# Kernel tuning notes

Measured on AMD Instinct MI355X. Metric: run time of the kernel, lower is better.

## Reference

```python
import jax, jax.numpy as jnp
import numpy as np

B = 8
N_PER = 8192   # xyz points per batch
M_PER = 2048   # query points per batch
C_FEAT = 32
RADIUS = 0.2
K = 32         # sample_nums
USE_XYZ = True


def setup_inputs() -> dict:
    key = jax.random.key(0)
    k1, k2, k3 = jax.random.split(key, 3)
    xyz = jax.random.uniform(k1, (B * N_PER, 3), dtype=jnp.float32)
    new_xyz = jax.random.uniform(k2, (B * M_PER, 3), dtype=jnp.float32)
    features = jax.random.normal(k3, (B * N_PER, C_FEAT), dtype=jnp.float32)
    xyz_batch_cnt = jnp.full((B,), N_PER, dtype=jnp.int32)
    new_xyz_batch_cnt = jnp.full((B,), M_PER, dtype=jnp.int32)
    return {
        "xyz": xyz,
        "xyz_batch_cnt": xyz_batch_cnt,
        "new_xyz": new_xyz,
        "new_xyz_batch_cnt": new_xyz_batch_cnt,
        "features": features,
    }


def _ball_query(xyz_b, new_b, radius, k):
    # xyz_b: (B, N, 3), new_b: (B, M, 3)
    n = xyz_b.shape[1]
    # squared pairwise distances (B, M, N)
    d2 = jnp.sum((new_b[:, :, None, :] - xyz_b[:, None, :, :]) ** 2, axis=-1)
    mask = d2 < (radius * radius)
    # first-k in-radius indices (CUDA ball_query keeps neighbors in point order)
    scores = jnp.where(mask, jnp.arange(n, dtype=jnp.int32), jnp.int32(n))
    idx_sorted = jnp.sort(scores, axis=-1)[..., :k]          # (B, M, k)
    cnt = jnp.sum(mask, axis=-1)                              # (B, M)
    empty = cnt == 0                                          # (B, M)
    first = idx_sorted[..., :1]                               # duplicate first hit
    slot = jnp.arange(k, dtype=jnp.int32)
    idx = jnp.where(slot[None, None, :] < cnt[..., None], idx_sorted, first)
    idx = jnp.where(empty[..., None], jnp.int32(0), idx)      # empty balls -> 0
    return idx, empty


def reference(xyz, xyz_batch_cnt, new_xyz, new_xyz_batch_cnt, features):
    b = xyz_batch_cnt.shape[0]
    xyz_b = xyz.reshape(b, -1, 3)          # (B, N, 3)
    new_b = new_xyz.reshape(b, -1, 3)      # (B, M, 3)
    feat_b = features.reshape(b, xyz_b.shape[1], -1)  # (B, N, C)

    idx, empty = _ball_query(xyz_b, new_b, RADIUS, K)  # (B, M, K), (B, M)

    gather = jax.vmap(lambda pts, i: pts[i])           # per-batch gather
    grouped_xyz = gather(xyz_b, idx) - new_b[:, :, None, :]   # (B, M, K, 3)
    grouped_xyz = jnp.where(empty[..., None, None], 0.0, grouped_xyz)

    grouped_feat = gather(feat_b, idx)                        # (B, M, K, C)
    grouped_feat = jnp.where(empty[..., None, None], 0.0, grouped_feat)

    if USE_XYZ:
        new_features = jnp.concatenate([grouped_xyz, grouped_feat], axis=-1)
    else:
        new_features = grouped_feat
    # (B, M, K, 3+C) -> (B*M, 3+C, K) to match torch (Mtot, C', nsample)
    m_tot = b * new_b.shape[1]
    new_features = jnp.transpose(new_features, (0, 1, 3, 2)).reshape(
        m_tot, -1, K)
    idx_flat = idx.reshape(m_tot, K)
    return new_features, idx_flat
```

## Files before the change

### kernel.cpp

```cpp
#include <hip/hip_runtime.h>

#define BATCHES   8
#define N_PER     8192
#define M_PER     2048
#define C_FEAT    32
#define KNN       32
#define R2        0.04f
#define M_TOT     (BATCHES * M_PER)
#define FEAT_OUT  (3 + C_FEAT)
#define OUT_FEAT_SZ ((size_t)M_TOT * FEAT_OUT * KNN)

__global__ __launch_bounds__(256) void sqag_fused_kernel(
    const float* __restrict__ xyz,
    const float* __restrict__ new_xyz,
    const float* __restrict__ features,
    float* __restrict__ out)
{
    __shared__ int sidx[4][KNN];

    const int wave = threadIdx.x >> 6;
    const int lane = threadIdx.x & 63;

    const int bswz   = blockIdx.x & 7;
    const int within = blockIdx.x >> 3;
    const int q = __builtin_amdgcn_readfirstlane(
        (bswz * (M_PER / 4) + within) * 4 + wave);
    const int b    = q >> 11;
    const int base = b * N_PER;

    const float px = new_xyz[q * 3 + 0];
    const float py = new_xyz[q * 3 + 1];
    const float pz = new_xyz[q * 3 + 2];

    int cnt = 0;
    int first = 0;

    float cx[4], cy[4], cz[4];
    const float* p = xyz + (size_t)base * 3 + lane * 3;
    #pragma unroll
    for (int c = 0; c < 4; ++c) {
        cx[c] = p[c * 192 + 0];
        cy[c] = p[c * 192 + 1];
        cz[c] = p[c * 192 + 2];
    }

    for (int cb = 0;;) {
        const bool more = (cb + 256) < N_PER;
        float nx[4], ny[4], nz[4];
        if (more) {
            const float* pn = p + 768;
            #pragma unroll
            for (int c = 0; c < 4; ++c) {
                nx[c] = pn[c * 192 + 0];
                ny[c] = pn[c * 192 + 1];
                nz[c] = pn[c * 192 + 2];
            }
        }

        unsigned long long m[4];
        bool in[4];
        #pragma unroll
        for (int c = 0; c < 4; ++c) {
            const float dx = px - cx[c];
            const float dy = py - cy[c];
            const float dz = pz - cz[c];
            const float d2 = __fadd_rn(__fadd_rn(__fmul_rn(dx, dx),
                                                 __fmul_rn(dy, dy)),
                                       __fmul_rn(dz, dz));
            in[c] = d2 < R2;
            m[c]  = __ballot(in[c]);
        }

        if (cnt == 0) {
            if      (m[0]) first = cb +       (__ffsll((long long)m[0]) - 1);
            else if (m[1]) first = cb +  64 + (__ffsll((long long)m[1]) - 1);
            else if (m[2]) first = cb + 128 + (__ffsll((long long)m[2]) - 1);
            else if (m[3]) first = cb + 192 + (__ffsll((long long)m[3]) - 1);
        }

        int pre = cnt;
        #pragma unroll
        for (int c = 0; c < 4; ++c) {
            if (in[c]) {
                const int r = pre + (int)__builtin_amdgcn_mbcnt_hi(
                    (unsigned)(m[c] >> 32),
                    __builtin_amdgcn_mbcnt_lo((unsigned)m[c], 0u));
                if (r < KNN) sidx[wave][r] = cb + c * 64 + lane;
            }
            pre += __popcll(m[c]);
        }
        cnt = pre;

        if (cnt >= KNN || !more) break;
        p += 768;
        cb += 256;
        #pragma unroll
        for (int c = 0; c < 4; ++c) {
            cx[c] = nx[c]; cy[c] = ny[c]; cz[c] = nz[c];
        }
    }

    const int pad = (cnt == 0) ? 0 : first;
    if (lane >= cnt && lane < KNN) sidx[wave][lane] = pad;
    const float zf = (cnt == 0) ? 0.0f : 1.0f;

    const int k    = lane & 31;
    const int half = lane >> 5;

    const int li = sidx[wave][k];
    const int gi = base + li;

    const float4* f = (const float4*)(features + (size_t)gi * C_FEAT + half * 16);
    const float4 v0 = f[0];
    const float4 v1 = f[1];
    const float4 v2 = f[2];
    const float4 v3 = f[3];

    const float gx = xyz[(size_t)gi * 3 + 0] - px;
    const float gy = xyz[(size_t)gi * 3 + 1] - py;
    const float gz = xyz[(size_t)gi * 3 + 2] - pz;

    float* o = out + (size_t)q * (FEAT_OUT * KNN);
    if (half == 0) {
        __builtin_nontemporal_store(zf * gx, &o[0 * KNN + k]);
        __builtin_nontemporal_store(zf * gy, &o[1 * KNN + k]);
        __builtin_nontemporal_store(zf * gz, &o[2 * KNN + k]);
        __builtin_nontemporal_store((float)li,
                                    &out[OUT_FEAT_SZ + (size_t)q * KNN + k]);
    }

    const int jb = 3 + half * 16;
    __builtin_nontemporal_store(zf * v0.x, &o[(jb +  0) * KNN + k]);
    __builtin_nontemporal_store(zf * v0.y, &o[(jb +  1) * KNN + k]);
    __builtin_nontemporal_store(zf * v0.z, &o[(jb +  2) * KNN + k]);
    __builtin_nontemporal_store(zf * v0.w, &o[(jb +  3) * KNN + k]);
    __builtin_nontemporal_store(zf * v1.x, &o[(jb +  4) * KNN + k]);
    __builtin_nontemporal_store(zf * v1.y, &o[(jb +  5) * KNN + k]);
    __builtin_nontemporal_store(zf * v1.z, &o[(jb +  6) * KNN + k]);
    __builtin_nontemporal_store(zf * v1.w, &o[(jb +  7) * KNN + k]);
    __builtin_nontemporal_store(zf * v2.x, &o[(jb +  8) * KNN + k]);
    __builtin_nontemporal_store(zf * v2.y, &o[(jb +  9) * KNN + k]);
    __builtin_nontemporal_store(zf * v2.z, &o[(jb + 10) * KNN + k]);
    __builtin_nontemporal_store(zf * v2.w, &o[(jb + 11) * KNN + k]);
    __builtin_nontemporal_store(zf * v3.x, &o[(jb + 12) * KNN + k]);
    __builtin_nontemporal_store(zf * v3.y, &o[(jb + 13) * KNN + k]);
    __builtin_nontemporal_store(zf * v3.z, &o[(jb + 14) * KNN + k]);
    __builtin_nontemporal_store(zf * v3.w, &o[(jb + 15) * KNN + k]);
}

extern "C" void kernel_launch(void* const* d_in, const int* in_sizes, int n_in,
                              void* d_out, int out_size, void* d_ws, size_t ws_size,
                              hipStream_t stream) {
    const float* xyz      = (const float*)d_in[0];
    const float* new_xyz  = (const float*)d_in[2];
    const float* features = (const float*)d_in[4];
    float* out = (float*)d_out;

    sqag_fused_kernel<<<M_TOT / 4, 256, 0, stream>>>(xyz, new_xyz, features, out);
}
```

Baseline: 115.6 us.

## Deepen xyz prefetch to two chunks and pack distance math into float2 ops

Extends the ball-query scan from a one-chunk to a two-chunk-ahead software prefetch of candidate coordinates, which hides more global load latency during the scan. It also packs pairs of candidate distance computations into 2-wide float vectors so the compiler can emit packed FP32 instructions. FMA contraction is disabled so results match the unfused reference rounding. This raises register use and issues extra loads that are wasted when the scan exits early.

```diff
diff --git a/kernel.cpp b/kernel.cpp
--- a/kernel.cpp
+++ b/kernel.cpp
@@ -10,12 +10,15 @@
 #define FEAT_OUT  (3 + C_FEAT)
 #define OUT_FEAT_SZ ((size_t)M_TOT * FEAT_OUT * KNN)
 
+typedef float v2f __attribute__((ext_vector_type(2)));
+
 __global__ __launch_bounds__(256) void sqag_fused_kernel(
     const float* __restrict__ xyz,
     const float* __restrict__ new_xyz,
     const float* __restrict__ features,
     float* __restrict__ out)
 {
+#pragma clang fp contract(off)
     __shared__ int sidx[4][KNN];
 
     const int wave = threadIdx.x >> 6;
@@ -31,44 +34,58 @@
     const float px = new_xyz[q * 3 + 0];
     const float py = new_xyz[q * 3 + 1];
     const float pz = new_xyz[q * 3 + 2];
+    const v2f px2 = {px, px}, py2 = {py, py}, pz2 = {pz, pz};
 
     int cnt = 0;
     int first = 0;
 
-    float cx[4], cy[4], cz[4];
+    v2f Ax[2], Ay[2], Az[2], Bx[2], By[2], Bz[2];
+
     const float* p = xyz + (size_t)base * 3 + lane * 3;
     #pragma unroll
-    for (int c = 0; c < 4; ++c) {
-        cx[c] = p[c * 192 + 0];
-        cy[c] = p[c * 192 + 1];
-        cz[c] = p[c * 192 + 2];
+    for (int h = 0; h < 2; ++h) {
+        Ax[h] = (v2f){p[h * 384 + 0],   p[h * 384 + 192]};
+        Ay[h] = (v2f){p[h * 384 + 1],   p[h * 384 + 193]};
+        Az[h] = (v2f){p[h * 384 + 2],   p[h * 384 + 194]};
+    }
+    {
+        const float* p1 = p + 768;
+        #pragma unroll
+        for (int h = 0; h < 2; ++h) {
+            Bx[h] = (v2f){p1[h * 384 + 0],   p1[h * 384 + 192]};
+            By[h] = (v2f){p1[h * 384 + 1],   p1[h * 384 + 193]};
+            Bz[h] = (v2f){p1[h * 384 + 2],   p1[h * 384 + 194]};
+        }
     }
 
     for (int cb = 0;;) {
-        const bool more = (cb + 256) < N_PER;
-        float nx[4], ny[4], nz[4];
-        if (more) {
-            const float* pn = p + 768;
+        v2f Cx[2], Cy[2], Cz[2];
+        const bool have2 = (cb + 512) < N_PER;
+        if (have2) {
+            const float* p2 = p + 1536;
             #pragma unroll
-            for (int c = 0; c < 4; ++c) {
-                nx[c] = pn[c * 192 + 0];
-                ny[c] = pn[c * 192 + 1];
-                nz[c] = pn[c * 192 + 2];
+            for (int h = 0; h < 2; ++h) {
+                Cx[h] = (v2f){p2[h * 384 + 0],   p2[h * 384 + 192]};
+                Cy[h] = (v2f){p2[h * 384 + 1],   p2[h * 384 + 193]};
+                Cz[h] = (v2f){p2[h * 384 + 2],   p2[h * 384 + 194]};
             }
         }
 
         unsigned long long m[4];
         bool in[4];
         #pragma unroll
-        for (int c = 0; c < 4; ++c) {
-            const float dx = px - cx[c];
-            const float dy = py - cy[c];
-            const float dz = pz - cz[c];
-            const float d2 = __fadd_rn(__fadd_rn(__fmul_rn(dx, dx),
-                                                 __fmul_rn(dy, dy)),
-                                       __fmul_rn(dz, dz));
-            in[c] = d2 < R2;
-            m[c]  = __ballot(in[c]);
+        for (int h = 0; h < 2; ++h) {
+            const v2f dx = px2 - Ax[h];
+            const v2f dy = py2 - Ay[h];
+            const v2f dz = pz2 - Az[h];
+            const v2f t  = dx * dx;
+            const v2f u  = dy * dy;
+            const v2f v  = dz * dz;
+            const v2f d2 = (t + u) + v;
+            in[h * 2 + 0] = d2.x < R2;
+            in[h * 2 + 1] = d2.y < R2;
+            m[h * 2 + 0]  = __ballot(in[h * 2 + 0]);
+            m[h * 2 + 1]  = __ballot(in[h * 2 + 1]);
         }
 
         if (cnt == 0) {
@@ -91,12 +108,13 @@
         }
         cnt = pre;
 
-        if (cnt >= KNN || !more) break;
+        if (cnt >= KNN || (cb + 256) >= N_PER) break;
         p += 768;
         cb += 256;
         #pragma unroll
-        for (int c = 0; c < 4; ++c) {
-            cx[c] = nx[c]; cy[c] = ny[c]; cz[c] = nz[c];
+        for (int h = 0; h < 2; ++h) {
+            Ax[h] = Bx[h]; Ay[h] = By[h]; Az[h] = Bz[h];
+            Bx[h] = Cx[h]; By[h] = Cy[h]; Bz[h] = Cz[h];
         }
     }
 
```

Measured after the change: 119.1 us. +3.0%, slower.
